# Kernel optimization log

Hardware: AMD Instinct MI355X
Metric: run time of the kernel (lower is better)

Reference implementation:

```python
import jax, jax.numpy as jnp
import numpy as np

DM = 1024        # model dim
E = 32           # totalexperts = expertsets*nexperts = 8*4
FE = 128         # expertsize
T = 4            # sparsity = nexperts (tokens per group)
EPS_TIEBREAK = 1e-6


def setup_inputs() -> dict:
    key = jax.random.key(0)
    k0, k1, k2, k3 = jax.random.split(key, 4)
    x = jax.random.normal(k0, (4, 4096, DM), dtype=jnp.float32)
    # fan_in-style inits matching misc.get_init_weight / get_init_bias
    controller = jax.random.normal(k1, (DM, E), dtype=jnp.float32) / np.float32(np.sqrt(DM))
    f1 = jax.random.normal(k2, (DM, E, FE), dtype=jnp.float32) / np.float32(np.sqrt(DM))
    bias = jnp.zeros((E, FE), dtype=jnp.float32)
    f2 = jax.random.normal(k3, (E, FE, DM), dtype=jnp.float32) / np.float32(np.sqrt(E * FE / T))
    return {"x": x, "controller": controller, "f1": f1, "bias": bias, "f2": f2}


def reference(x, controller, f1, bias, f2):
    B, S, d = x.shape
    t = T
    g = S // t
    # '... (b t) d -> ... b t d'
    grouped = x.reshape(B, g, t, d)
    # controller logits: '... t d, d e -> ... t e'
    logits = jnp.einsum('bgtd,de->bgte', grouped, controller)
    # deterministic tie-break offset over the t (slot) axis
    logits = logits + jnp.linspace(0.0, EPS_TIEBREAK, t, dtype=logits.dtype)[:, None]
    # softmax over dim=1 (group axis) as in original
    probs = jax.nn.softmax(logits, axis=1)
    # hard argmax mask over dim=-3 (group axis), scaled by soft probs
    perm = (logits == jnp.max(logits, axis=1, keepdims=True)).astype(x.dtype) * probs
    # expert up-projection with soft permutation: '... t d, d e f, ... t e -> ... e f'
    inner = jnp.einsum('bgtd,def,bgte->bgef', grouped, f1, perm)
    inner = jax.nn.relu(inner + bias)
    # expert down-projection: '... e f, e f d -> ... e d'
    inter = jnp.einsum('bgef,efd->bged', inner, f2)
    # unpermute: '... e d, ... t e -> ... t d'
    res = jnp.einsum('bged,bgte->bgtd', inter, perm)
    return res.reshape(B, S, d)
```

## Files before the change

kernel.cpp:

```cpp
#include <hip/hip_runtime.h>
#include <math.h>


#define DM   1024
#define NE   32
#define FE   128
#define T4   4
#define SS   4096
#define NGRP 1024
#define NROW 512
#define LP_STRIDE (NROW * NGRP)
#define VP_OFF   524288

__global__ __launch_bounds__(256, 2)
void k_logits(const float* __restrict__ x, const float* __restrict__ ctrl,
              float* __restrict__ Lp, float* __restrict__ out)
{
    const int m      = blockIdx.x;
    const int ks     = blockIdx.y;
    const int tid    = threadIdx.x;
    const int base_s = m * 128;
    const int b      = base_s >> 12;
    const int g0     = (base_s & 4095) >> 2;

    __shared__ float xT[64 * 132];
    __shared__ float cs[64 * 32];

    const int tq = tid & 31;
    const int eg = tid >> 5;

    float acc[4][4];
#pragma unroll
    for (int i = 0; i < 4; ++i)
#pragma unroll
        for (int j = 0; j < 4; ++j) acc[i][j] = 0.f;

    const int row0 = tid >> 2;
    const int f4i  = tid & 3;

    float4 px[2][4];
    float4 pc[2];

    {
        const int k0 = ks * 256;
#pragma unroll
        for (int rr = 0; rr < 2; ++rr) {
            const float* xp = x + (size_t)(base_s + row0 + rr * 64) * DM + k0;
#pragma unroll
            for (int cr = 0; cr < 4; ++cr)
                px[rr][cr] = *(const float4*)(xp + (f4i + cr * 4) * 4);
        }
        const float4* cg = (const float4*)(ctrl + (size_t)k0 * NE);
        pc[0] = cg[tid]; pc[1] = cg[tid + 256];
    }

    for (int kit = 0; kit < 4; ++kit) {
        __syncthreads();
#pragma unroll
        for (int rr = 0; rr < 2; ++rr) {
            const int row = row0 + rr * 64;
#pragma unroll
            for (int cr = 0; cr < 4; ++cr) {
                const int d = (f4i + cr * 4) * 4;
                const float4 v = px[rr][cr];
                xT[(d + 0) * 132 + row] = v.x;
                xT[(d + 1) * 132 + row] = v.y;
                xT[(d + 2) * 132 + row] = v.z;
                xT[(d + 3) * 132 + row] = v.w;
            }
        }
        {
            float4* cl = (float4*)cs;
            cl[tid] = pc[0]; cl[tid + 256] = pc[1];
        }
        __syncthreads();

        if (kit < 3) {
            const int k0 = ks * 256 + (kit + 1) * 64;
#pragma unroll
            for (int rr = 0; rr < 2; ++rr) {
                const float* xp = x + (size_t)(base_s + row0 + rr * 64) * DM + k0;
#pragma unroll
                for (int cr = 0; cr < 4; ++cr)
                    px[rr][cr] = *(const float4*)(xp + (f4i + cr * 4) * 4);
            }
            const float4* cg = (const float4*)(ctrl + (size_t)k0 * NE);
            pc[0] = cg[tid]; pc[1] = cg[tid + 256];
        }

#pragma unroll 4
        for (int d = 0; d < 64; ++d) {
            const float4 xv = *(const float4*)(xT + d * 132 + tq * 4);
            const float4 cv = *(const float4*)(cs + d * 32 + eg * 4);
            const float xa[4] = { xv.x, xv.y, xv.z, xv.w };
            const float ca[4] = { cv.x, cv.y, cv.z, cv.w };
#pragma unroll
            for (int i = 0; i < 4; ++i)
#pragma unroll
                for (int j = 0; j < 4; ++j) acc[i][j] += xa[i] * ca[j];
        }
    }

    {
        float* Lb = Lp + (size_t)ks * LP_STRIDE;
        const int g = g0 + tq;
#pragma unroll
        for (int i = 0; i < 4; ++i)
#pragma unroll
            for (int j = 0; j < 4; ++j) {
                const int row = (b * T4 + i) * NE + eg * 4 + j;
                Lb[(size_t)row * NGRP + g] = acc[i][j];
            }
    }

    {
        const float4 z = make_float4(0.f, 0.f, 0.f, 0.f);
        float4* o4 = (float4*)(out + (size_t)(base_s + ks * 32) * DM);
#pragma unroll 4
        for (int i = tid; i < 32 * DM / 4; i += 256) o4[i] = z;
    }
}

__global__ __launch_bounds__(64)
void k_route(float* __restrict__ Lp)
{
    const int r    = blockIdx.x;
    const int lane = threadIdx.x;
    const float* L0 = Lp + (size_t)r * NGRP;

    float mx = -INFINITY, s = 0.f;
    int gm = 0;
#pragma unroll
    for (int c = 0; c < 4; ++c) {
        const int g0c = c * 256 + lane * 4;
        const float4 v0 = *(const float4*)(L0 + g0c);
        const float4 v1 = *(const float4*)(L0 + 1 * LP_STRIDE + g0c);
        const float4 v2 = *(const float4*)(L0 + 2 * LP_STRIDE + g0c);
        const float4 v3 = *(const float4*)(L0 + 3 * LP_STRIDE + g0c);
        const float l[4] = { v0.x + v1.x + v2.x + v3.x,
                             v0.y + v1.y + v2.y + v3.y,
                             v0.z + v1.z + v2.z + v3.z,
                             v0.w + v1.w + v2.w + v3.w };
#pragma unroll
        for (int j = 0; j < 4; ++j) {
            const float lv = l[j];
            if (lv > mx) { s = s * __expf(mx - lv) + 1.f; mx = lv; gm = g0c + j; }
            else         { s += __expf(lv - mx); }
        }
    }
#pragma unroll
    for (int off = 1; off < 64; off <<= 1) {
        const float m2 = __shfl_xor(mx, off);
        const float s2 = __shfl_xor(s, off);
        const int   g2 = __shfl_xor(gm, off);
        const float mn = fmaxf(mx, m2);
        s  = s * __expf(mx - mn) + s2 * __expf(m2 - mn);
        gm = (m2 > mx) ? g2 : ((m2 == mx && g2 < gm) ? g2 : gm);
        mx = mn;
    }
    if (lane == 0) {
        ((int*)Lp)[(size_t)r * NGRP] = gm;
        Lp[(size_t)r * NGRP + 1] = 1.f / s;
    }
}

__global__ __launch_bounds__(256, 4)
void k_up(const float* __restrict__ x, const float* __restrict__ f1,
          float* __restrict__ ws)
{
    const int e   = blockIdx.x & 31;
    const int dc  = (blockIdx.x >> 5) & 15;
    const int rh  = blockIdx.x >> 9;
    const int tid = threadIdx.x;

    __shared__ float xs[8 * 68];
    __shared__ int   gS[8];

    if (tid < 8) {
        const int r = (rh * 8 + tid) * NE + e;
        gS[tid] = ((const int*)ws)[(size_t)r * NGRP];
    }
    __syncthreads();

    if (tid < 128) {
        const int row = tid >> 4;
        const int f4c = tid & 15;
        const int grow = rh * 8 + row;
        const int bq = grow >> 2, t = grow & 3;
        const int s = bq * SS + gS[row] * 4 + t;
        const float4 v = *(const float4*)(x + (size_t)s * DM + dc * 64 + f4c * 4);
        xs[row * 68 + f4c * 4 + 0] = v.x;
        xs[row * 68 + f4c * 4 + 1] = v.y;
        xs[row * 68 + f4c * 4 + 2] = v.z;
        xs[row * 68 + f4c * 4 + 3] = v.w;
    }
    __syncthreads();

    const int f4 = tid & 31;
    const int rw = tid >> 5;
    const float* f1p = f1 + (size_t)(dc * 64) * (NE * FE) + e * FE + f4 * 4;
    const float* xp  = xs + rw * 68;

    float a[4] = {0.f, 0.f, 0.f, 0.f};
#pragma unroll 16
    for (int dl = 0; dl < 64; ++dl) {
        const float4 w4 = *(const float4*)(f1p + (size_t)dl * (NE * FE));
        const float xa = xp[dl];
        a[0] += xa * w4.x; a[1] += xa * w4.y; a[2] += xa * w4.z; a[3] += xa * w4.w;
    }

    float* Vp = ws + VP_OFF + (size_t)(dc * 32 + e) * (16 * FE);
    *(float4*)(Vp + (rh * 8 + rw) * FE + f4 * 4) = make_float4(a[0], a[1], a[2], a[3]);
}

__global__ __launch_bounds__(256, 2)
void k_down(const float* __restrict__ f2, const float* __restrict__ bias,
            const float* __restrict__ ws, float* __restrict__ out)
{
    const int e   = blockIdx.x & 31;
    const int dt  = (blockIdx.x >> 5) & 7;
    const int rh  = blockIdx.x >> 8;
    const int tid = threadIdx.x;

    __shared__ float vv[8 * 132];
    __shared__ float hs[8 * 132];
    __shared__ int   gS[8];
    __shared__ float pS[8];

    if (tid < 8) {
        const int r = (rh * 8 + tid) * NE + e;
        gS[tid] = ((const int*)ws)[(size_t)r * NGRP];
        pS[tid] = ws[(size_t)r * NGRP + 1];
    }

    {
        const float* Vp = ws + VP_OFF;
        const int row = tid >> 5, f4 = tid & 31;
        float4 s = make_float4(0.f, 0.f, 0.f, 0.f);
#pragma unroll
        for (int dc = 0; dc < 16; ++dc) {
            const float4 v = *(const float4*)(Vp + (size_t)(dc * 32 + e) * (16 * FE)
                                                 + (rh * 8 + row) * FE + f4 * 4);
            s.x += v.x; s.y += v.y; s.z += v.z; s.w += v.w;
        }
        *(float4*)(vv + row * 132 + f4 * 4) = s;
    }
    __syncthreads();

    {
#pragma unroll
        for (int q = 0; q < 4; ++q) {
            const int idx = tid + q * 256;
            const int row = idx >> 7, f = idx & 127;
            const int qb = row & ~3;
            float u = bias[e * FE + f];
#pragma unroll
            for (int t2 = 0; t2 < T4; ++t2)
                if (gS[qb + t2] == gS[row]) u += pS[qb + t2] * vv[(qb + t2) * 132 + f];
            hs[row * 132 + f] = pS[row] * fmaxf(u, 0.f);
        }
    }
    __syncthreads();

    const int d4 = tid & 31;
    const int rw = tid >> 5;
    const float* f2p = f2 + (size_t)e * FE * DM + dt * 128 + d4 * 4;
    const float* hp  = hs + rw * 132;

    float a[4] = {0.f, 0.f, 0.f, 0.f};
#pragma unroll 16
    for (int f = 0; f < FE; ++f) {
        const float4 w4 = *(const float4*)(f2p + (size_t)f * DM);
        const float ha = hp[f];
        a[0] += ha * w4.x; a[1] += ha * w4.y; a[2] += ha * w4.z; a[3] += ha * w4.w;
    }

    const int grow = rh * 8 + rw;
    const int bq = grow >> 2, t = grow & 3;
    float* orow = out + ((size_t)(bq * SS + gS[rw] * 4 + t)) * DM + dt * 128 + d4 * 4;
    atomicAdd(orow + 0, a[0]);
    atomicAdd(orow + 1, a[1]);
    atomicAdd(orow + 2, a[2]);
    atomicAdd(orow + 3, a[3]);
}

extern "C" void kernel_launch(void* const* d_in, const int* in_sizes, int n_in,
                              void* d_out, int out_size, void* d_ws, size_t ws_size,
                              hipStream_t stream)
{
    const float* x    = (const float*)d_in[0];
    const float* ctrl = (const float*)d_in[1];
    const float* f1   = (const float*)d_in[2];
    const float* bias = (const float*)d_in[3];
    const float* f2   = (const float*)d_in[4];
    float* out = (float*)d_out;
    float* ws  = (float*)d_ws;

    k_logits<<<dim3(128, 4), 256, 0, stream>>>(x, ctrl, ws, out);
    k_route <<<dim3(512),     64, 0, stream>>>(ws);
    k_up    <<<dim3(1024),   256, 0, stream>>>(x, f1, ws);
    k_down  <<<dim3(512),    256, 0, stream>>>(f2, bias, ws, out);
}
```

Before: 199.7 us.

## Widen per-thread register tiles in logits and up-projection kernels

k_logits now runs 128 threads per block, each computing a 4x8 logits tile instead of 4x4. It drops the register-prefetch double buffering and loads tiles straight into shared memory. k_up processes all 16 routed rows per block, so each f1 weight load is reused for two rows and the f1 traffic is halved, with half as many blocks. The aims are fewer redundant weight reads and more work per thread. The costs are less latency hiding in k_logits and lower occupancy and parallelism in both kernels.

```diff
diff --git a/kernel.cpp b/kernel.cpp
--- a/kernel.cpp
+++ b/kernel.cpp
@@ -12,7 +12,7 @@
 #define LP_STRIDE (NROW * NGRP)
 #define VP_OFF   524288
 
-__global__ __launch_bounds__(256, 2)
+__global__ __launch_bounds__(128, 2)
 void k_logits(const float* __restrict__ x, const float* __restrict__ ctrl,
               float* __restrict__ Lp, float* __restrict__ out)
 {
@@ -29,75 +29,49 @@
     const int tq = tid & 31;
     const int eg = tid >> 5;
 
-    float acc[4][4];
+    float acc[4][8];
 #pragma unroll
     for (int i = 0; i < 4; ++i)
 #pragma unroll
-        for (int j = 0; j < 4; ++j) acc[i][j] = 0.f;
-
-    const int row0 = tid >> 2;
-    const int f4i  = tid & 3;
-
-    float4 px[2][4];
-    float4 pc[2];
-
-    {
-        const int k0 = ks * 256;
-#pragma unroll
-        for (int rr = 0; rr < 2; ++rr) {
-            const float* xp = x + (size_t)(base_s + row0 + rr * 64) * DM + k0;
-#pragma unroll
-            for (int cr = 0; cr < 4; ++cr)
-                px[rr][cr] = *(const float4*)(xp + (f4i + cr * 4) * 4);
-        }
-        const float4* cg = (const float4*)(ctrl + (size_t)k0 * NE);
-        pc[0] = cg[tid]; pc[1] = cg[tid + 256];
-    }
+        for (int j = 0; j < 8; ++j) acc[i][j] = 0.f;
+
+    const int srow = tid >> 4;
+    const int scol = tid & 15;
 
     for (int kit = 0; kit < 4; ++kit) {
+        const int k0 = ks * 256 + kit * 64;
         __syncthreads();
 #pragma unroll
-        for (int rr = 0; rr < 2; ++rr) {
-            const int row = row0 + rr * 64;
-#pragma unroll
-            for (int cr = 0; cr < 4; ++cr) {
-                const int d = (f4i + cr * 4) * 4;
-                const float4 v = px[rr][cr];
-                xT[(d + 0) * 132 + row] = v.x;
-                xT[(d + 1) * 132 + row] = v.y;
-                xT[(d + 2) * 132 + row] = v.z;
-                xT[(d + 3) * 132 + row] = v.w;
-            }
+        for (int p = 0; p < 16; ++p) {
+            const int row = p * 8 + srow;
+            const float4 v = *(const float4*)(x + (size_t)(base_s + row) * DM + k0 + scol * 4);
+            const int d = scol * 4;
+            xT[(d + 0) * 132 + row] = v.x;
+            xT[(d + 1) * 132 + row] = v.y;
+            xT[(d + 2) * 132 + row] = v.z;
+            xT[(d + 3) * 132 + row] = v.w;
         }
         {
+            const float4* cg = (const float4*)(ctrl + (size_t)k0 * NE);
             float4* cl = (float4*)cs;
-            cl[tid] = pc[0]; cl[tid + 256] = pc[1];
+            cl[tid]       = cg[tid];
+            cl[tid + 128] = cg[tid + 128];
+            cl[tid + 256] = cg[tid + 256];
+            cl[tid + 384] = cg[tid + 384];
         }
         __syncthreads();
-
-        if (kit < 3) {
-            const int k0 = ks * 256 + (kit + 1) * 64;
-#pragma unroll
-            for (int rr = 0; rr < 2; ++rr) {
-                const float* xp = x + (size_t)(base_s + row0 + rr * 64) * DM + k0;
-#pragma unroll
-                for (int cr = 0; cr < 4; ++cr)
-                    px[rr][cr] = *(const float4*)(xp + (f4i + cr * 4) * 4);
-            }
-            const float4* cg = (const float4*)(ctrl + (size_t)k0 * NE);
-            pc[0] = cg[tid]; pc[1] = cg[tid + 256];
-        }
 
 #pragma unroll 4
         for (int d = 0; d < 64; ++d) {
             const float4 xv = *(const float4*)(xT + d * 132 + tq * 4);
-            const float4 cv = *(const float4*)(cs + d * 32 + eg * 4);
+            const float4 c0 = *(const float4*)(cs + d * 32 + eg * 8);
+            const float4 c1 = *(const float4*)(cs + d * 32 + eg * 8 + 4);
             const float xa[4] = { xv.x, xv.y, xv.z, xv.w };
-            const float ca[4] = { cv.x, cv.y, cv.z, cv.w };
+            const float ca[8] = { c0.x, c0.y, c0.z, c0.w, c1.x, c1.y, c1.z, c1.w };
 #pragma unroll
             for (int i = 0; i < 4; ++i)
 #pragma unroll
-                for (int j = 0; j < 4; ++j) acc[i][j] += xa[i] * ca[j];
+                for (int j = 0; j < 8; ++j) acc[i][j] += xa[i] * ca[j];
         }
     }
 
@@ -107,8 +81,8 @@
 #pragma unroll
         for (int i = 0; i < 4; ++i)
 #pragma unroll
-            for (int j = 0; j < 4; ++j) {
-                const int row = (b * T4 + i) * NE + eg * 4 + j;
+            for (int j = 0; j < 8; ++j) {
+                const int row = (b * T4 + i) * NE + eg * 8 + j;
                 Lb[(size_t)row * NGRP + g] = acc[i][j];
             }
     }
@@ -116,8 +90,8 @@
     {
         const float4 z = make_float4(0.f, 0.f, 0.f, 0.f);
         float4* o4 = (float4*)(out + (size_t)(base_s + ks * 32) * DM);
-#pragma unroll 4
-        for (int i = tid; i < 32 * DM / 4; i += 256) o4[i] = z;
+#pragma unroll 8
+        for (int i = tid; i < 32 * DM / 4; i += 128) o4[i] = z;
     }
 }
 
@@ -164,29 +138,27 @@
     }
 }
 
-__global__ __launch_bounds__(256, 4)
+__global__ __launch_bounds__(256, 2)
 void k_up(const float* __restrict__ x, const float* __restrict__ f1,
           float* __restrict__ ws)
 {
     const int e   = blockIdx.x & 31;
-    const int dc  = (blockIdx.x >> 5) & 15;
-    const int rh  = blockIdx.x >> 9;
+    const int dc  = blockIdx.x >> 5;
     const int tid = threadIdx.x;
 
-    __shared__ float xs[8 * 68];
-    __shared__ int   gS[8];
-
-    if (tid < 8) {
-        const int r = (rh * 8 + tid) * NE + e;
+    __shared__ float xs[16 * 68];
+    __shared__ int   gS[16];
+
+    if (tid < 16) {
+        const int r = tid * NE + e;
         gS[tid] = ((const int*)ws)[(size_t)r * NGRP];
     }
     __syncthreads();
 
-    if (tid < 128) {
+    {
         const int row = tid >> 4;
         const int f4c = tid & 15;
-        const int grow = rh * 8 + row;
-        const int bq = grow >> 2, t = grow & 3;
+        const int bq = row >> 2, t = row & 3;
         const int s = bq * SS + gS[row] * 4 + t;
         const float4 v = *(const float4*)(x + (size_t)s * DM + dc * 64 + f4c * 4);
         xs[row * 68 + f4c * 4 + 0] = v.x;
@@ -199,18 +171,21 @@
     const int f4 = tid & 31;
     const int rw = tid >> 5;
     const float* f1p = f1 + (size_t)(dc * 64) * (NE * FE) + e * FE + f4 * 4;
-    const float* xp  = xs + rw * 68;
-
-    float a[4] = {0.f, 0.f, 0.f, 0.f};
+    const float* x0 = xs + rw * 68;
+    const float* x1 = xs + (rw + 8) * 68;
+
+    float a0[4] = {0.f, 0.f, 0.f, 0.f}, a1[4] = {0.f, 0.f, 0.f, 0.f};
 #pragma unroll 16
     for (int dl = 0; dl < 64; ++dl) {
         const float4 w4 = *(const float4*)(f1p + (size_t)dl * (NE * FE));
-        const float xa = xp[dl];
-        a[0] += xa * w4.x; a[1] += xa * w4.y; a[2] += xa * w4.z; a[3] += xa * w4.w;
+        const float xa = x0[dl], xb = x1[dl];
+        a0[0] += xa * w4.x; a0[1] += xa * w4.y; a0[2] += xa * w4.z; a0[3] += xa * w4.w;
+        a1[0] += xb * w4.x; a1[1] += xb * w4.y; a1[2] += xb * w4.z; a1[3] += xb * w4.w;
     }
 
     float* Vp = ws + VP_OFF + (size_t)(dc * 32 + e) * (16 * FE);
-    *(float4*)(Vp + (rh * 8 + rw) * FE + f4 * 4) = make_float4(a[0], a[1], a[2], a[3]);
+    *(float4*)(Vp + rw       * FE + f4 * 4) = make_float4(a0[0], a0[1], a0[2], a0[3]);
+    *(float4*)(Vp + (rw + 8) * FE + f4 * 4) = make_float4(a1[0], a1[1], a1[2], a1[3]);
 }
 
 __global__ __launch_bounds__(256, 2)
@@ -296,8 +271,8 @@
     float* out = (float*)d_out;
     float* ws  = (float*)d_ws;
 
-    k_logits<<<dim3(128, 4), 256, 0, stream>>>(x, ctrl, ws, out);
+    k_logits<<<dim3(128, 4), 128, 0, stream>>>(x, ctrl, ws, out);
     k_route <<<dim3(512),     64, 0, stream>>>(ws);
-    k_up    <<<dim3(1024),   256, 0, stream>>>(x, f1, ws);
+    k_up    <<<dim3(512),    256, 0, stream>>>(x, f1, ws);
     k_down  <<<dim3(512),    256, 0, stream>>>(f2, bias, ws, out);
 }
```

Result: no change. 202.3 us (+1.3%).
